# Performance work log

Hardware: AMD Instinct MI355X
Metric: run time of the kernel (lower is better)

## Reference

```python
import jax, jax.numpy as jnp
import numpy as np

S, B, I, H, L, O = 2048, 64, 64, 128, 2, 1


def _lstm_dir(xs, w_ih, w_hh, b, reverse):
    # xs: (S, B, in); w_ih: (4H, in); w_hh: (4H, H); b: (4H,) = b_ih + b_hh
    # PyTorch gate order: i, f, g, o
    gx = jnp.einsum('sbi,gi->sbg', xs, w_ih) + b  # precompute input gates once
    h0 = jnp.zeros((xs.shape[1], w_hh.shape[1]), xs.dtype)
    c0 = jnp.zeros_like(h0)

    def step(carry, g_t):
        h, c = carry
        g = g_t + h @ w_hh.T
        i, f, gg, o = jnp.split(g, 4, axis=-1)
        i = jax.nn.sigmoid(i)
        f = jax.nn.sigmoid(f)
        gg = jnp.tanh(gg)
        o = jax.nn.sigmoid(o)
        c = f * c + i * gg
        h = o * jnp.tanh(c)
        return (h, c), h

    _, hs = jax.lax.scan(step, (h0, c0), gx, reverse=reverse)
    return hs  # (S, B, H), time-aligned for both directions (PyTorch semantics)


def _bilstm(x, layers):
    out = x
    for (wif, whf, bf, wir, whr, br) in layers:
        hf = _lstm_dir(out, wif, whf, bf, reverse=False)
        hb = _lstm_dir(out, wir, whr, br, reverse=True)
        out = jnp.concatenate([hf, hb], axis=-1)  # (S, B, 2H)
    return out


def setup_inputs() -> dict:
    key = jax.random.key(0)
    ks = jax.random.split(key, 16)
    sc = 1.0 / np.sqrt(H)
    u = lambda k, shp: jax.random.uniform(k, shp, jnp.float32, -sc, sc)
    inp = {
        'x': jax.random.normal(ks[0], (S, B, I), jnp.float32),
        # layer 0 (input size I)
        'w_ih_f0': u(ks[1], (4 * H, I)), 'w_hh_f0': u(ks[2], (4 * H, H)), 'b_f0': u(ks[3], (4 * H,)),
        'w_ih_r0': u(ks[4], (4 * H, I)), 'w_hh_r0': u(ks[5], (4 * H, H)), 'b_r0': u(ks[6], (4 * H,)),
        # layer 1 (input size 2H)
        'w_ih_f1': u(ks[7], (4 * H, 2 * H)), 'w_hh_f1': u(ks[8], (4 * H, H)), 'b_f1': u(ks[9], (4 * H,)),
        'w_ih_r1': u(ks[10], (4 * H, 2 * H)), 'w_hh_r1': u(ks[11], (4 * H, H)), 'b_r1': u(ks[12], (4 * H,)),
        # final linear: (O, 2H), (O,)
        'w_out': u(ks[13], (O, 2 * H)), 'b_out': u(ks[14], (O,)),
    }
    return inp


def reference(x, w_ih_f0, w_hh_f0, b_f0, w_ih_r0, w_hh_r0, b_r0,
              w_ih_f1, w_hh_f1, b_f1, w_ih_r1, w_hh_r1, b_r1, w_out, b_out):
    layers = [
        (w_ih_f0, w_hh_f0, b_f0, w_ih_r0, w_hh_r0, b_r0),
        (w_ih_f1, w_hh_f1, b_f1, w_ih_r1, w_hh_r1, b_r1),
    ]
    h = _bilstm(x, layers)                      # (S, B, 2H)
    y = jnp.einsum('sbh,oh->sbo', h, w_out) + b_out  # linear over flattened (s*b, h)
    return y
```

## Files before the change

### kernel.cpp

```cpp
#include <hip/hip_runtime.h>
#include <hip/hip_bf16.h>

#define SEQ 2048
#define NB  64

typedef _Float16 f16x8 __attribute__((ext_vector_type(8)));
typedef _Float16 f16x4 __attribute__((ext_vector_type(4)));
typedef float    f32x4 __attribute__((ext_vector_type(4)));

__device__ __forceinline__ float fast_sigmoid(float x) {
    float e = __builtin_amdgcn_exp2f(-1.4426950408889634f * x);
    return __builtin_amdgcn_rcpf(1.f + e);
}
__device__ __forceinline__ float fast_tanh(float x) {
    float e = __builtin_amdgcn_exp2f(2.8853900817779268f * x);
    return fmaf(-2.f, __builtin_amdgcn_rcpf(1.f + e), 1.f);
}

__global__ __launch_bounds__(256) void split_f32(
    const float* __restrict__ s, _Float16* __restrict__ hi,
    _Float16* __restrict__ lo, int n)
{
    int i = blockIdx.x * 256 + threadIdx.x;
    if (i < n) {
        float v = s[i];
        _Float16 h = (_Float16)v;
        hi[i] = h;
        lo[i] = (_Float16)(v - (float)h);
    }
}


__global__ __launch_bounds__(256) void gemm0(
    const float* __restrict__ x,
    const _Float16* __restrict__ whi_f, const _Float16* __restrict__ wlo_f,
    const _Float16* __restrict__ whi_r, const _Float16* __restrict__ wlo_r,
    const float* __restrict__ bf_, const float* __restrict__ br_,
    float* __restrict__ gx, int tq0)
{
    const int lane = threadIdx.x & 63, wave = threadIdx.x >> 6;
    const int dir  = blockIdx.z;
    const _Float16* Whi = dir ? whi_r : whi_f;
    const _Float16* Wlo = dir ? wlo_r : wlo_f;
    const float* bias   = dir ? br_   : bf_;
    const int s   = blockIdx.y;
    const int t   = dir ? (SEQ - 1 - tq0 - s) : (tq0 + s);
    const int n0  = blockIdx.x * 64;
    const int col = lane & 15, kg = lane >> 4;

    f32x4 acc[4] = {{0,0,0,0},{0,0,0,0},{0,0,0,0},{0,0,0,0}};
    #pragma unroll
    for (int ks = 0; ks < 2; ++ks) {
        const float* ar = x + ((size_t)t*NB + wave*16 + col) * 64 + ks*32 + kg*8;
        float4 a0 = *(const float4*)ar;
        float4 a1 = *(const float4*)(ar + 4);
        f16x8 ahi, alo;
        float av[8] = {a0.x,a0.y,a0.z,a0.w,a1.x,a1.y,a1.z,a1.w};
        #pragma unroll
        for (int e = 0; e < 8; ++e) {
            _Float16 h = (_Float16)av[e];
            ahi[e] = h; alo[e] = (_Float16)(av[e] - (float)h);
        }
        #pragma unroll
        for (int nt = 0; nt < 4; ++nt) {
            size_t idx = (size_t)(n0 + nt*16 + col) * 64 + ks*32 + kg*8;
            f16x8 bhi = *(const f16x8*)(Whi + idx);
            f16x8 blo = *(const f16x8*)(Wlo + idx);
            acc[nt] = __builtin_amdgcn_mfma_f32_16x16x32_f16(ahi, bhi, acc[nt], 0,0,0);
            acc[nt] = __builtin_amdgcn_mfma_f32_16x16x32_f16(ahi, blo, acc[nt], 0,0,0);
            acc[nt] = __builtin_amdgcn_mfma_f32_16x16x32_f16(alo, bhi, acc[nt], 0,0,0);
        }
    }
    #pragma unroll
    for (int nt = 0; nt < 4; ++nt) {
        const int n = n0 + nt*16 + col;
        const float bv = bias[n];
        f32x4 v = {acc[nt][0]+bv, acc[nt][1]+bv, acc[nt][2]+bv, acc[nt][3]+bv};
        size_t fi = (size_t)s*65536 + (size_t)(dir*4 + wave)*8192
                  + (size_t)(blockIdx.x*4 + nt)*256 + lane*4;
        *(f32x4*)(gx + fi) = v;
    }
}

template<int SPLIT_A>
__global__ __launch_bounds__(256) void gemm1(
    const _Float16* __restrict__ Ahi, const _Float16* __restrict__ Alo,
    const _Float16* __restrict__ whi_f, const _Float16* __restrict__ wlo_f,
    const _Float16* __restrict__ whi_r, const _Float16* __restrict__ wlo_r,
    const float* __restrict__ bf_, const float* __restrict__ br_,
    float* __restrict__ gx, int tq0)
{
    const int lane = threadIdx.x & 63, wave = threadIdx.x >> 6;
    const int dir  = blockIdx.z;
    const _Float16* Whi = dir ? whi_r : whi_f;
    const _Float16* Wlo = dir ? wlo_r : wlo_f;
    const float* bias   = dir ? br_   : bf_;
    const int wm = wave >> 1, wn = wave & 1;
    const int s  = blockIdx.y;
    const int t  = dir ? (SEQ - 1 - tq0 - s) : (tq0 + s);
    const int n0 = blockIdx.x * 64 + wn * 32;
    const int col = lane & 15, kg = lane >> 4;

    f32x4 acc[2][2] = {{{0,0,0,0},{0,0,0,0}},{{0,0,0,0},{0,0,0,0}}};
    #pragma unroll
    for (int ks = 0; ks < 8; ++ks) {
        f16x8 ahi[2], alo[2];
        #pragma unroll
        for (int mt = 0; mt < 2; ++mt) {
            const size_t arow = (size_t)t*NB + wm*32 + mt*16 + col;
            ahi[mt] = *(const f16x8*)(Ahi + arow*256 + ks*32 + kg*8);
            if constexpr (SPLIT_A) alo[mt] = *(const f16x8*)(Alo + arow*256 + ks*32 + kg*8);
        }
        #pragma unroll
        for (int nt = 0; nt < 2; ++nt) {
            size_t idx = (size_t)(n0 + nt*16 + col) * 256 + ks*32 + kg*8;
            f16x8 bhi = *(const f16x8*)(Whi + idx);
            f16x8 blo = *(const f16x8*)(Wlo + idx);
            #pragma unroll
            for (int mt = 0; mt < 2; ++mt) {
                acc[mt][nt] = __builtin_amdgcn_mfma_f32_16x16x32_f16(ahi[mt], bhi, acc[mt][nt], 0,0,0);
                acc[mt][nt] = __builtin_amdgcn_mfma_f32_16x16x32_f16(ahi[mt], blo, acc[mt][nt], 0,0,0);
                if constexpr (SPLIT_A)
                    acc[mt][nt] = __builtin_amdgcn_mfma_f32_16x16x32_f16(alo[mt], bhi, acc[mt][nt], 0,0,0);
            }
        }
    }
    #pragma unroll
    for (int mt = 0; mt < 2; ++mt)
        #pragma unroll
        for (int nt = 0; nt < 2; ++nt) {
            const int n = n0 + nt*16 + col;
            const float bv = bias[n];
            f32x4 v = {acc[mt][nt][0]+bv, acc[mt][nt][1]+bv, acc[mt][nt][2]+bv, acc[mt][nt][3]+bv};
            size_t fi = (size_t)s*65536 + (size_t)(dir*4 + (wm*2+mt))*8192
                      + (size_t)(blockIdx.x*4 + wn*2 + nt)*256 + lane*4;
            *(f32x4*)(gx + fi) = v;
        }
}

template<int OMODE>
__global__ __launch_bounds__(512, 2) void lstm_rec3(
    const float* __restrict__ gx,
    const float* __restrict__ Whf, const float* __restrict__ Whr,
    _Float16* __restrict__ o1, _Float16* __restrict__ o2,
    float* __restrict__ state,
    int tq0, int steps, int first)
{
    const int bg  = blockIdx.x;
    const int dir = blockIdx.y;
    const float* Wh = dir ? Whr : Whf;
    const int tid  = threadIdx.x;
    const int w    = tid >> 6;
    const int lane = tid & 63;
    const int col  = lane & 15;
    const int kg   = lane >> 4;
    const int kidx = 16*w + col;

    f16x8 Bhi[4][4], Blo[4][4];
    #pragma unroll
    for (int T = 0; T < 4; ++T) {
        const float* wr = Wh + (size_t)((8*T + w)*16 + col) * 128;
        #pragma unroll
        for (int ks = 0; ks < 4; ++ks) {
            const float* p4 = wr + ks*32 + kg*8;
            float4 a0 = *(const float4*)p4, a1 = *(const float4*)(p4+4);
            float av[8] = {a0.x,a0.y,a0.z,a0.w,a1.x,a1.y,a1.z,a1.w};
            f16x8 hi, lo;
            #pragma unroll
            for (int e = 0; e < 8; ++e) {
                _Float16 h = (_Float16)av[e];
                hi[e] = h; lo[e] = (_Float16)(av[e] - (float)h);
            }
            Bhi[T][ks] = hi; Blo[T][ks] = lo;
        }
    }

    __shared__ f16x8 HhiA[256], HloA[256], HhiB[256], HloB[256];

    float cr[4], hr[4];
    float* stbase = state + ((size_t)dir*4 + bg) * 4096;
    #pragma unroll
    for (int r = 0; r < 4; ++r) {
        const int m = kg*4 + r;
        float hv = first ? 0.f : stbase[m*128 + kidx];
        float cv = first ? 0.f : stbase[2048 + m*128 + kidx];
        hr[r] = hv; cr[r] = cv;
        _Float16 hhi = (_Float16)hv;
        _Float16 hlo = (_Float16)(hv - (float)hhi);
        const int el = m*128 + (((kidx>>3) ^ m) & 15)*8 + (kidx & 7);
        ((_Float16*)HhiA)[el] = hhi;
        ((_Float16*)HloA)[el] = hlo;
    }
    __syncthreads();

    const float* gxp = gx + (size_t)(dir*4 + bg)*8192 + (size_t)lane*4;

    f32x4 gA[4], gB[4];
    #pragma unroll
    for (int T = 0; T < 4; ++T) {
        gA[T] = *(const f32x4*)(gxp + (8*T + w)*256);
        gB[T] = *(const f32x4*)(gxp + (8*T + w)*256 + 65536);
    }

    auto rec_step = [&](f32x4 (&G)[4], f16x8 (&RHI)[256], f16x8 (&RLO)[256],
                        f16x8 (&WHI)[256], f16x8 (&WLO)[256], int STEP) {
        f16x8 Ah[4], Al[4];
        #pragma unroll
        for (int ks = 0; ks < 4; ++ks) {
            const int u = col*16 + ((ks*4 + kg) ^ col);
            Ah[ks] = RHI[u];
            Al[ks] = RLO[u];
        }
        f32x4 acc0 = G[0], acc1 = G[1], acc2 = G[2], acc3 = G[3];
        #pragma unroll
        for (int T = 0; T < 4; ++T)
            G[T] = *(const f32x4*)(gxp + (8*T + w)*256 + (size_t)(STEP + 2)*65536);
        #pragma unroll
        for (int ks = 0; ks < 4; ++ks) {
            acc0 = __builtin_amdgcn_mfma_f32_16x16x32_f16(Ah[ks], Bhi[0][ks], acc0, 0,0,0);
            acc0 = __builtin_amdgcn_mfma_f32_16x16x32_f16(Al[ks], Bhi[0][ks], acc0, 0,0,0);
            acc0 = __builtin_amdgcn_mfma_f32_16x16x32_f16(Ah[ks], Blo[0][ks], acc0, 0,0,0);
            acc1 = __builtin_amdgcn_mfma_f32_16x16x32_f16(Ah[ks], Bhi[1][ks], acc1, 0,0,0);
            acc1 = __builtin_amdgcn_mfma_f32_16x16x32_f16(Al[ks], Bhi[1][ks], acc1, 0,0,0);
            acc1 = __builtin_amdgcn_mfma_f32_16x16x32_f16(Ah[ks], Blo[1][ks], acc1, 0,0,0);
            acc2 = __builtin_amdgcn_mfma_f32_16x16x32_f16(Ah[ks], Bhi[2][ks], acc2, 0,0,0);
            acc2 = __builtin_amdgcn_mfma_f32_16x16x32_f16(Al[ks], Bhi[2][ks], acc2, 0,0,0);
            acc2 = __builtin_amdgcn_mfma_f32_16x16x32_f16(Ah[ks], Blo[2][ks], acc2, 0,0,0);
            acc3 = __builtin_amdgcn_mfma_f32_16x16x32_f16(Ah[ks], Bhi[3][ks], acc3, 0,0,0);
            acc3 = __builtin_amdgcn_mfma_f32_16x16x32_f16(Al[ks], Bhi[3][ks], acc3, 0,0,0);
            acc3 = __builtin_amdgcn_mfma_f32_16x16x32_f16(Ah[ks], Blo[3][ks], acc3, 0,0,0);
        }
        const int t = dir ? (SEQ-1 - tq0 - STEP) : (tq0 + STEP);
        #pragma unroll
        for (int r = 0; r < 4; ++r) {
            float iv = fast_sigmoid(acc0[r]);
            float fv = fast_sigmoid(acc1[r]);
            float gv = fast_tanh(acc2[r]);
            float ov = fast_sigmoid(acc3[r]);
            float cv = fmaf(fv, cr[r], iv * gv);
            cr[r] = cv;
            float hv = ov * fast_tanh(cv);
            hr[r] = hv;
            _Float16 hhi = (_Float16)hv;
            _Float16 hlo = (_Float16)(hv - (float)hhi);
            const int m = kg*4 + r;
            const int el = m*128 + (((kidx>>3) ^ m) & 15)*8 + (kidx & 7);
            ((_Float16*)WHI)[el] = hhi;
            ((_Float16*)WLO)[el] = hlo;
            const size_t oi = ((size_t)t*NB + (bg*16 + m))*256 + dir*128 + kidx;
            o1[oi] = hhi;
            if constexpr (OMODE == 0) o2[oi] = hlo;
        }
        asm volatile("s_waitcnt lgkmcnt(0)" ::: "memory");
        __builtin_amdgcn_s_barrier();
        asm volatile("" ::: "memory");
    };

    for (int step = 0; step < steps; step += 2) {
        rec_step(gA, HhiA, HloA, HhiB, HloB, step);
        rec_step(gB, HhiB, HloB, HhiA, HloA, step + 1);
    }

    #pragma unroll
    for (int r = 0; r < 4; ++r) {
        const int m = kg*4 + r;
        stbase[m*128 + kidx] = hr[r];
        stbase[2048 + m*128 + kidx] = cr[r];
    }
}

__global__ __launch_bounds__(256) void final_lin(
    const _Float16* __restrict__ out1,
    const float* __restrict__ wout, const float* __restrict__ bout,
    float* __restrict__ y)
{
    const int lane = threadIdx.x & 63;
    const int wave = threadIdx.x >> 6;
    const int row  = blockIdx.x * 4 + wave;
    f16x4 u = *(const f16x4*)(out1 + (size_t)row*256 + lane*4);
    float4 wv = *(const float4*)(wout + lane*4);
    float s = (float)u[0]*wv.x + (float)u[1]*wv.y + (float)u[2]*wv.z + (float)u[3]*wv.w;
    #pragma unroll
    for (int off = 32; off > 0; off >>= 1) s += __shfl_down(s, off, 64);
    if (lane == 0) y[row] = s + bout[0];
}

extern "C" void kernel_launch(void* const* d_in, const int* in_sizes, int n_in,
                              void* d_out, int out_size, void* d_ws, size_t ws_size,
                              hipStream_t stream) {
    const float* x      = (const float*)d_in[0];
    const float* wih_f0 = (const float*)d_in[1];
    const float* whh_f0 = (const float*)d_in[2];
    const float* b_f0   = (const float*)d_in[3];
    const float* wih_r0 = (const float*)d_in[4];
    const float* whh_r0 = (const float*)d_in[5];
    const float* b_r0   = (const float*)d_in[6];
    const float* wih_f1 = (const float*)d_in[7];
    const float* whh_f1 = (const float*)d_in[8];
    const float* b_f1   = (const float*)d_in[9];
    const float* wih_r1 = (const float*)d_in[10];
    const float* whh_r1 = (const float*)d_in[11];
    const float* b_r1   = (const float*)d_in[12];
    const float* w_out  = (const float*)d_in[13];
    const float* b_out  = (const float*)d_in[14];

    const size_t w0N = 512*64, w1N = (size_t)512*256;
    const size_t w0B = w0N*2, w1B = w1N*2;
    const size_t stB = 2*4*4096*4;
    const size_t hB  = (size_t)SEQ*NB*256*2;
    const size_t fixedB = 4*w0B + 4*w1B + stB;

    const int cand[7] = {2048, 1024, 512, 256, 128, 64, 32};
    int Tc = 0; int tierA = 1;
    for (int i = 0; i < 7 && !Tc; ++i)
        if (fixedB + 3*hB + (size_t)(cand[i]+2)*65536*4 <= ws_size) Tc = cand[i];
    if (!Tc) {
        tierA = 0;
        for (int i = 0; i < 7 && !Tc; ++i)
            if (fixedB + 2*hB + (size_t)(cand[i]+2)*65536*4 <= ws_size) Tc = cand[i];
        if (!Tc) Tc = 32;
    }
    const int nq = SEQ / Tc;

    char* p = (char*)d_ws;
    _Float16* whi0f = (_Float16*)p; p += w0B;
    _Float16* wlo0f = (_Float16*)p; p += w0B;
    _Float16* whi0r = (_Float16*)p; p += w0B;
    _Float16* wlo0r = (_Float16*)p; p += w0B;
    _Float16* whi1f = (_Float16*)p; p += w1B;
    _Float16* wlo1f = (_Float16*)p; p += w1B;
    _Float16* whi1r = (_Float16*)p; p += w1B;
    _Float16* wlo1r = (_Float16*)p; p += w1B;
    float*    state = (float*)p;    p += stB;
    _Float16* out1  = (_Float16*)p; p += hB;
    _Float16* h0hi  = (_Float16*)p; p += hB;
    _Float16* h0lo  = (_Float16*)p; if (tierA) p += hB;
    float*    gx    = (float*)p;

    split_f32<<<(int)((w0N+255)/256), 256, 0, stream>>>(wih_f0, whi0f, wlo0f, (int)w0N);
    split_f32<<<(int)((w0N+255)/256), 256, 0, stream>>>(wih_r0, whi0r, wlo0r, (int)w0N);
    split_f32<<<(int)((w1N+255)/256), 256, 0, stream>>>(wih_f1, whi1f, wlo1f, (int)w1N);
    split_f32<<<(int)((w1N+255)/256), 256, 0, stream>>>(wih_r1, whi1r, wlo1r, (int)w1N);

    for (int q = 0; q < nq; ++q) {
        gemm0<<<dim3(8, Tc, 2), 256, 0, stream>>>(x, whi0f, wlo0f, whi0r, wlo0r,
                                                  b_f0, b_r0, gx, q*Tc);
        if (tierA)
            lstm_rec3<0><<<dim3(4,2), 512, 0, stream>>>(gx, whh_f0, whh_r0, h0hi, h0lo,
                                                        state, q*Tc, Tc, q==0);
        else
            lstm_rec3<1><<<dim3(4,2), 512, 0, stream>>>(gx, whh_f0, whh_r0, h0hi, nullptr,
                                                        state, q*Tc, Tc, q==0);
    }
    for (int q = 0; q < nq; ++q) {
        if (tierA)
            gemm1<1><<<dim3(8, Tc, 2), 256, 0, stream>>>(h0hi, h0lo, whi1f, wlo1f, whi1r, wlo1r,
                                                         b_f1, b_r1, gx, q*Tc);
        else
            gemm1<0><<<dim3(8, Tc, 2), 256, 0, stream>>>(h0hi, h0hi, whi1f, wlo1f, whi1r, wlo1r,
                                                         b_f1, b_r1, gx, q*Tc);
        lstm_rec3<1><<<dim3(4,2), 512, 0, stream>>>(gx, whh_f1, whh_r1, out1, nullptr,
                                                    state, q*Tc, Tc, q==0);
    }
    final_lin<<<SEQ*NB/4, 256, 0, stream>>>(out1, w_out, b_out, (float*)d_out);
}
```

Before: 6.886 ms.

## Overlap next-chunk input GEMM with recurrence via combined megastep kernel launch

Merges the input-projection GEMM and the LSTM recurrence into one kernel launch. The first 8 blocks run the recurrence on the current chunk while the remaining blocks compute gate inputs for the next chunk into a double-buffered gx. The goal is to hide the GEMM work behind the latency-bound recurrence that occupies only 8 blocks. It also fuses the four weight-split launches into one, caps the chunk size at 256, and drops the low-memory fallback tier, so the full hi/lo buffers are now always required. The trade-off is more kernel launches from the smaller chunks and GEMM blocks that may contend with the recurrence blocks for CUs.

```diff
diff --git a/kernel.cpp b/kernel.cpp
--- a/kernel.cpp
+++ b/kernel.cpp
@@ -17,137 +17,35 @@
     return fmaf(-2.f, __builtin_amdgcn_rcpf(1.f + e), 1.f);
 }
 
-__global__ __launch_bounds__(256) void split_f32(
-    const float* __restrict__ s, _Float16* __restrict__ hi,
-    _Float16* __restrict__ lo, int n)
+__global__ __launch_bounds__(256) void split_all(
+    const float* __restrict__ w0f, const float* __restrict__ w0r,
+    const float* __restrict__ w1f, const float* __restrict__ w1r,
+    _Float16* hi0f, _Float16* lo0f, _Float16* hi0r, _Float16* lo0r,
+    _Float16* hi1f, _Float16* lo1f, _Float16* hi1r, _Float16* lo1r)
 {
-    int i = blockIdx.x * 256 + threadIdx.x;
-    if (i < n) {
-        float v = s[i];
-        _Float16 h = (_Float16)v;
-        hi[i] = h;
-        lo[i] = (_Float16)(v - (float)h);
-    }
-}
-
-
-__global__ __launch_bounds__(256) void gemm0(
-    const float* __restrict__ x,
-    const _Float16* __restrict__ whi_f, const _Float16* __restrict__ wlo_f,
-    const _Float16* __restrict__ whi_r, const _Float16* __restrict__ wlo_r,
-    const float* __restrict__ bf_, const float* __restrict__ br_,
-    float* __restrict__ gx, int tq0)
-{
-    const int lane = threadIdx.x & 63, wave = threadIdx.x >> 6;
-    const int dir  = blockIdx.z;
-    const _Float16* Whi = dir ? whi_r : whi_f;
-    const _Float16* Wlo = dir ? wlo_r : wlo_f;
-    const float* bias   = dir ? br_   : bf_;
-    const int s   = blockIdx.y;
-    const int t   = dir ? (SEQ - 1 - tq0 - s) : (tq0 + s);
-    const int n0  = blockIdx.x * 64;
-    const int col = lane & 15, kg = lane >> 4;
-
-    f32x4 acc[4] = {{0,0,0,0},{0,0,0,0},{0,0,0,0},{0,0,0,0}};
-    #pragma unroll
-    for (int ks = 0; ks < 2; ++ks) {
-        const float* ar = x + ((size_t)t*NB + wave*16 + col) * 64 + ks*32 + kg*8;
-        float4 a0 = *(const float4*)ar;
-        float4 a1 = *(const float4*)(ar + 4);
-        f16x8 ahi, alo;
-        float av[8] = {a0.x,a0.y,a0.z,a0.w,a1.x,a1.y,a1.z,a1.w};
-        #pragma unroll
-        for (int e = 0; e < 8; ++e) {
-            _Float16 h = (_Float16)av[e];
-            ahi[e] = h; alo[e] = (_Float16)(av[e] - (float)h);
-        }
-        #pragma unroll
-        for (int nt = 0; nt < 4; ++nt) {
-            size_t idx = (size_t)(n0 + nt*16 + col) * 64 + ks*32 + kg*8;
-            f16x8 bhi = *(const f16x8*)(Whi + idx);
-            f16x8 blo = *(const f16x8*)(Wlo + idx);
-            acc[nt] = __builtin_amdgcn_mfma_f32_16x16x32_f16(ahi, bhi, acc[nt], 0,0,0);
-            acc[nt] = __builtin_amdgcn_mfma_f32_16x16x32_f16(ahi, blo, acc[nt], 0,0,0);
-            acc[nt] = __builtin_amdgcn_mfma_f32_16x16x32_f16(alo, bhi, acc[nt], 0,0,0);
-        }
-    }
-    #pragma unroll
-    for (int nt = 0; nt < 4; ++nt) {
-        const int n = n0 + nt*16 + col;
-        const float bv = bias[n];
-        f32x4 v = {acc[nt][0]+bv, acc[nt][1]+bv, acc[nt][2]+bv, acc[nt][3]+bv};
-        size_t fi = (size_t)s*65536 + (size_t)(dir*4 + wave)*8192
-                  + (size_t)(blockIdx.x*4 + nt)*256 + lane*4;
-        *(f32x4*)(gx + fi) = v;
-    }
-}
-
-template<int SPLIT_A>
-__global__ __launch_bounds__(256) void gemm1(
-    const _Float16* __restrict__ Ahi, const _Float16* __restrict__ Alo,
-    const _Float16* __restrict__ whi_f, const _Float16* __restrict__ wlo_f,
-    const _Float16* __restrict__ whi_r, const _Float16* __restrict__ wlo_r,
-    const float* __restrict__ bf_, const float* __restrict__ br_,
-    float* __restrict__ gx, int tq0)
-{
-    const int lane = threadIdx.x & 63, wave = threadIdx.x >> 6;
-    const int dir  = blockIdx.z;
-    const _Float16* Whi = dir ? whi_r : whi_f;
-    const _Float16* Wlo = dir ? wlo_r : wlo_f;
-    const float* bias   = dir ? br_   : bf_;
-    const int wm = wave >> 1, wn = wave & 1;
-    const int s  = blockIdx.y;
-    const int t  = dir ? (SEQ - 1 - tq0 - s) : (tq0 + s);
-    const int n0 = blockIdx.x * 64 + wn * 32;
-    const int col = lane & 15, kg = lane >> 4;
-
-    f32x4 acc[2][2] = {{{0,0,0,0},{0,0,0,0}},{{0,0,0,0},{0,0,0,0}}};
-    #pragma unroll
-    for (int ks = 0; ks < 8; ++ks) {
-        f16x8 ahi[2], alo[2];
-        #pragma unroll
-        for (int mt = 0; mt < 2; ++mt) {
-            const size_t arow = (size_t)t*NB + wm*32 + mt*16 + col;
-            ahi[mt] = *(const f16x8*)(Ahi + arow*256 + ks*32 + kg*8);
-            if constexpr (SPLIT_A) alo[mt] = *(const f16x8*)(Alo + arow*256 + ks*32 + kg*8);
-        }
-        #pragma unroll
-        for (int nt = 0; nt < 2; ++nt) {
-            size_t idx = (size_t)(n0 + nt*16 + col) * 256 + ks*32 + kg*8;
-            f16x8 bhi = *(const f16x8*)(Whi + idx);
-            f16x8 blo = *(const f16x8*)(Wlo + idx);
-            #pragma unroll
-            for (int mt = 0; mt < 2; ++mt) {
-                acc[mt][nt] = __builtin_amdgcn_mfma_f32_16x16x32_f16(ahi[mt], bhi, acc[mt][nt], 0,0,0);
-                acc[mt][nt] = __builtin_amdgcn_mfma_f32_16x16x32_f16(ahi[mt], blo, acc[mt][nt], 0,0,0);
-                if constexpr (SPLIT_A)
-                    acc[mt][nt] = __builtin_amdgcn_mfma_f32_16x16x32_f16(alo[mt], bhi, acc[mt][nt], 0,0,0);
-            }
-        }
-    }
-    #pragma unroll
-    for (int mt = 0; mt < 2; ++mt)
-        #pragma unroll
-        for (int nt = 0; nt < 2; ++nt) {
-            const int n = n0 + nt*16 + col;
-            const float bv = bias[n];
-            f32x4 v = {acc[mt][nt][0]+bv, acc[mt][nt][1]+bv, acc[mt][nt][2]+bv, acc[mt][nt][3]+bv};
-            size_t fi = (size_t)s*65536 + (size_t)(dir*4 + (wm*2+mt))*8192
-                      + (size_t)(blockIdx.x*4 + wn*2 + nt)*256 + lane*4;
-            *(f32x4*)(gx + fi) = v;
-        }
-}
-
-template<int OMODE>
-__global__ __launch_bounds__(512, 2) void lstm_rec3(
+    const int n0 = 512*64, n1 = 512*256;
+    int j = blockIdx.x * 256 + threadIdx.x;
+    const float* s; _Float16 *hi, *lo;
+    if (j < n0)                { s = w0f; hi = hi0f; lo = lo0f; }
+    else if ((j -= n0) < n0)   { s = w0r; hi = hi0r; lo = lo0r; }
+    else if ((j -= n0) < n1)   { s = w1f; hi = hi1f; lo = lo1f; }
+    else if ((j -= n1) < n1)   { s = w1r; hi = hi1r; lo = lo1r; }
+    else return;
+    float v = s[j];
+    _Float16 h = (_Float16)v;
+    hi[j] = h;
+    lo[j] = (_Float16)(v - (float)h);
+}
+
+
+template<int PHASE>
+__device__ __forceinline__ void rec_body(
     const float* __restrict__ gx,
     const float* __restrict__ Whf, const float* __restrict__ Whr,
     _Float16* __restrict__ o1, _Float16* __restrict__ o2,
-    float* __restrict__ state,
-    int tq0, int steps, int first)
+    float* __restrict__ state, int tq0, int steps, int first,
+    int bg, int dir)
 {
-    const int bg  = blockIdx.x;
-    const int dir = blockIdx.y;
     const float* Wh = dir ? Whr : Whf;
     const int tid  = threadIdx.x;
     const int w    = tid >> 6;
@@ -249,7 +147,7 @@
             ((_Float16*)WLO)[el] = hlo;
             const size_t oi = ((size_t)t*NB + (bg*16 + m))*256 + dir*128 + kidx;
             o1[oi] = hhi;
-            if constexpr (OMODE == 0) o2[oi] = hlo;
+            if constexpr (PHASE == 0) o2[oi] = hlo;
         }
         asm volatile("s_waitcnt lgkmcnt(0)" ::: "memory");
         __builtin_amdgcn_s_barrier();
@@ -266,6 +164,120 @@
         const int m = kg*4 + r;
         stbase[m*128 + kidx] = hr[r];
         stbase[2048 + m*128 + kidx] = cr[r];
+    }
+}
+
+template<int PHASE>
+__global__ __launch_bounds__(512, 2) void megastep(
+    const void* __restrict__ Agm, const _Float16* __restrict__ AloG,
+    const _Float16* __restrict__ whiF, const _Float16* __restrict__ wloF,
+    const _Float16* __restrict__ whiR, const _Float16* __restrict__ wloR,
+    const float* __restrict__ bF, const float* __restrict__ bR,
+    float* __restrict__ gxW,
+    const float* __restrict__ gxR,
+    const float* __restrict__ Whf, const float* __restrict__ Whr,
+    _Float16* __restrict__ o1, _Float16* __restrict__ o2,
+    float* __restrict__ state,
+    int nrec, int tq0r, int steps, int first,
+    int tq0g, int Tc)
+{
+    const int bid = blockIdx.x;
+    if (bid < nrec) {
+        rec_body<PHASE>(gxR, Whf, Whr, o1, o2, state, tq0r, steps, first,
+                        bid & 3, bid >> 2);
+        return;
+    }
+    const int g    = bid - nrec;
+    const int nblk = g & 7;
+    const int rr   = g >> 3;
+    const int half = Tc >> 1;
+    const int spair = rr % half;
+    const int dir   = rr / half;
+    const int tid  = threadIdx.x;
+    const int lane = tid & 63;
+    const int w8   = tid >> 6;
+    const int s    = spair*2 + (w8 >> 2);
+    const int wave = w8 & 3;
+    const int t    = dir ? (SEQ - 1 - tq0g - s) : (tq0g + s);
+    const _Float16* Whi = dir ? whiR : whiF;
+    const _Float16* Wlo = dir ? wloR : wloF;
+    const float* bias   = dir ? bR   : bF;
+    const int col = lane & 15, kg = lane >> 4;
+
+    if constexpr (PHASE == 0) {
+        const float* x = (const float*)Agm;
+        const int n0 = nblk * 64;
+        f32x4 acc[4] = {{0,0,0,0},{0,0,0,0},{0,0,0,0},{0,0,0,0}};
+        #pragma unroll
+        for (int ks = 0; ks < 2; ++ks) {
+            const float* ar = x + ((size_t)t*NB + wave*16 + col) * 64 + ks*32 + kg*8;
+            float4 a0 = *(const float4*)ar;
+            float4 a1 = *(const float4*)(ar + 4);
+            f16x8 ahi, alo;
+            float av[8] = {a0.x,a0.y,a0.z,a0.w,a1.x,a1.y,a1.z,a1.w};
+            #pragma unroll
+            for (int e = 0; e < 8; ++e) {
+                _Float16 h = (_Float16)av[e];
+                ahi[e] = h; alo[e] = (_Float16)(av[e] - (float)h);
+            }
+            #pragma unroll
+            for (int nt = 0; nt < 4; ++nt) {
+                size_t idx = (size_t)(n0 + nt*16 + col) * 64 + ks*32 + kg*8;
+                f16x8 bhi = *(const f16x8*)(Whi + idx);
+                f16x8 blo = *(const f16x8*)(Wlo + idx);
+                acc[nt] = __builtin_amdgcn_mfma_f32_16x16x32_f16(ahi, bhi, acc[nt], 0,0,0);
+                acc[nt] = __builtin_amdgcn_mfma_f32_16x16x32_f16(ahi, blo, acc[nt], 0,0,0);
+                acc[nt] = __builtin_amdgcn_mfma_f32_16x16x32_f16(alo, bhi, acc[nt], 0,0,0);
+            }
+        }
+        #pragma unroll
+        for (int nt = 0; nt < 4; ++nt) {
+            const int n = n0 + nt*16 + col;
+            const float bv = bias[n];
+            f32x4 v = {acc[nt][0]+bv, acc[nt][1]+bv, acc[nt][2]+bv, acc[nt][3]+bv};
+            size_t fi = (size_t)s*65536 + (size_t)(dir*4 + wave)*8192
+                      + (size_t)(nblk*4 + nt)*256 + lane*4;
+            *(f32x4*)(gxW + fi) = v;
+        }
+    } else {
+        const _Float16* Ahi = (const _Float16*)Agm;
+        const int wm = wave >> 1, wn = wave & 1;
+        const int n0 = nblk * 64 + wn * 32;
+        f32x4 acc[2][2] = {{{0,0,0,0},{0,0,0,0}},{{0,0,0,0},{0,0,0,0}}};
+        #pragma unroll
+        for (int ks = 0; ks < 8; ++ks) {
+            f16x8 ahi[2], alo[2];
+            #pragma unroll
+            for (int mt = 0; mt < 2; ++mt) {
+                const size_t arow = (size_t)t*NB + wm*32 + mt*16 + col;
+                ahi[mt] = *(const f16x8*)(Ahi  + arow*256 + ks*32 + kg*8);
+                alo[mt] = *(const f16x8*)(AloG + arow*256 + ks*32 + kg*8);
+            }
+            #pragma unroll
+            for (int nt = 0; nt < 2; ++nt) {
+                size_t idx = (size_t)(n0 + nt*16 + col) * 256 + ks*32 + kg*8;
+                f16x8 bhi = *(const f16x8*)(Whi + idx);
+                f16x8 blo = *(const f16x8*)(Wlo + idx);
+                #pragma unroll
+                for (int mt = 0; mt < 2; ++mt) {
+                    acc[mt][nt] = __builtin_amdgcn_mfma_f32_16x16x32_f16(ahi[mt], bhi, acc[mt][nt], 0,0,0);
+                    acc[mt][nt] = __builtin_amdgcn_mfma_f32_16x16x32_f16(ahi[mt], blo, acc[mt][nt], 0,0,0);
+                    acc[mt][nt] = __builtin_amdgcn_mfma_f32_16x16x32_f16(alo[mt], bhi, acc[mt][nt], 0,0,0);
+                }
+            }
+        }
+        #pragma unroll
+        for (int mt = 0; mt < 2; ++mt)
+            #pragma unroll
+            for (int nt = 0; nt < 2; ++nt) {
+                const int n = n0 + nt*16 + col;
+                const float bv = bias[n];
+                f32x4 v = {acc[mt][nt][0]+bv, acc[mt][nt][1]+bv,
+                           acc[mt][nt][2]+bv, acc[mt][nt][3]+bv};
+                size_t fi = (size_t)s*65536 + (size_t)(dir*4 + (wm*2+mt))*8192
+                          + (size_t)(nblk*4 + wn*2 + nt)*256 + lane*4;
+                *(f32x4*)(gxW + fi) = v;
+            }
     }
 }
 
@@ -308,18 +320,13 @@
     const size_t w0B = w0N*2, w1B = w1N*2;
     const size_t stB = 2*4*4096*4;
     const size_t hB  = (size_t)SEQ*NB*256*2;
+    const size_t gxStepB = 65536ull*4;
     const size_t fixedB = 4*w0B + 4*w1B + stB;
 
-    const int cand[7] = {2048, 1024, 512, 256, 128, 64, 32};
-    int Tc = 0; int tierA = 1;
-    for (int i = 0; i < 7 && !Tc; ++i)
-        if (fixedB + 3*hB + (size_t)(cand[i]+2)*65536*4 <= ws_size) Tc = cand[i];
-    if (!Tc) {
-        tierA = 0;
-        for (int i = 0; i < 7 && !Tc; ++i)
-            if (fixedB + 2*hB + (size_t)(cand[i]+2)*65536*4 <= ws_size) Tc = cand[i];
-        if (!Tc) Tc = 32;
-    }
+    const int cand[4] = {256, 128, 64, 32};
+    int Tc = 32;
+    for (int i = 0; i < 4; ++i)
+        if (fixedB + 3*hB + 2*(size_t)(cand[i]+2)*gxStepB <= ws_size) { Tc = cand[i]; break; }
     const int nq = SEQ / Tc;
 
     char* p = (char*)d_ws;
@@ -334,33 +341,38 @@
     float*    state = (float*)p;    p += stB;
     _Float16* out1  = (_Float16*)p; p += hB;
     _Float16* h0hi  = (_Float16*)p; p += hB;
-    _Float16* h0lo  = (_Float16*)p; if (tierA) p += hB;
-    float*    gx    = (float*)p;
-
-    split_f32<<<(int)((w0N+255)/256), 256, 0, stream>>>(wih_f0, whi0f, wlo0f, (int)w0N);
-    split_f32<<<(int)((w0N+255)/256), 256, 0, stream>>>(wih_r0, whi0r, wlo0r, (int)w0N);
-    split_f32<<<(int)((w1N+255)/256), 256, 0, stream>>>(wih_f1, whi1f, wlo1f, (int)w1N);
-    split_f32<<<(int)((w1N+255)/256), 256, 0, stream>>>(wih_r1, whi1r, wlo1r, (int)w1N);
-
+    _Float16* h0lo  = (_Float16*)p; p += hB;
+    float*    gx0   = (float*)p;    p += (size_t)(Tc+2)*gxStepB;
+    float*    gx1   = (float*)p;
+
+    split_all<<<(int)((2*w0N + 2*w1N + 255)/256), 256, 0, stream>>>(
+        wih_f0, wih_r0, wih_f1, wih_r1,
+        whi0f, wlo0f, whi0r, wlo0r, whi1f, wlo1f, whi1r, wlo1r);
+
+    const int ngemm = 8 * Tc;
+    float* gxb[2] = {gx0, gx1};
+
+    megastep<0><<<ngemm, 512, 0, stream>>>(
+        x, nullptr, whi0f, wlo0f, whi0r, wlo0r, b_f0, b_r0,
+        gxb[0], nullptr, nullptr, nullptr, nullptr, nullptr, nullptr,
+        0, 0, 0, 0, 0, Tc);
     for (int q = 0; q < nq; ++q) {
-        gemm0<<<dim3(8, Tc, 2), 256, 0, stream>>>(x, whi0f, wlo0f, whi0r, wlo0r,
-                                                  b_f0, b_r0, gx, q*Tc);
-        if (tierA)
-            lstm_rec3<0><<<dim3(4,2), 512, 0, stream>>>(gx, whh_f0, whh_r0, h0hi, h0lo,
-                                                        state, q*Tc, Tc, q==0);
-        else
-            lstm_rec3<1><<<dim3(4,2), 512, 0, stream>>>(gx, whh_f0, whh_r0, h0hi, nullptr,
-                                                        state, q*Tc, Tc, q==0);
-    }
+        const int nxt = (q + 1 < nq);
+        megastep<0><<<8 + (nxt ? ngemm : 0), 512, 0, stream>>>(
+            x, nullptr, whi0f, wlo0f, whi0r, wlo0r, b_f0, b_r0,
+            gxb[(q+1)&1], gxb[q&1], whh_f0, whh_r0, h0hi, h0lo, state,
+            8, q*Tc, Tc, q==0, (q+1)*Tc, Tc);
+    }
+    megastep<1><<<ngemm, 512, 0, stream>>>(
+        h0hi, h0lo, whi1f, wlo1f, whi1r, wlo1r, b_f1, b_r1,
+        gxb[0], nullptr, nullptr, nullptr, nullptr, nullptr, nullptr,
+        0, 0, 0, 0, 0, Tc);
     for (int q = 0; q < nq; ++q) {
-        if (tierA)
-            gemm1<1><<<dim3(8, Tc, 2), 256, 0, stream>>>(h0hi, h0lo, whi1f, wlo1f, whi1r, wlo1r,
-                                                         b_f1, b_r1, gx, q*Tc);
-        else
-            gemm1<0><<<dim3(8, Tc, 2), 256, 0, stream>>>(h0hi, h0hi, whi1f, wlo1f, whi1r, wlo1r,
-                                                         b_f1, b_r1, gx, q*Tc);
-        lstm_rec3<1><<<dim3(4,2), 512, 0, stream>>>(gx, whh_f1, whh_r1, out1, nullptr,
-                                                    state, q*Tc, Tc, q==0);
+        const int nxt = (q + 1 < nq);
+        megastep<1><<<8 + (nxt ? ngemm : 0), 512, 0, stream>>>(
+            h0hi, h0lo, whi1f, wlo1f, whi1r, wlo1r, b_f1, b_r1,
+            gxb[(q+1)&1], gxb[q&1], whh_f1, whh_r1, out1, nullptr, state,
+            8, q*Tc, Tc, q==0, (q+1)*Tc, Tc);
     }
     final_lin<<<SEQ*NB/4, 256, 0, stream>>>(out1, w_out, b_out, (float*)d_out);
 }
```

Result: faster. 5.953 ms (-13.5%).
